# Optimization experiments

Hardware: AMD Instinct MI355X
Metric: run time of the kernel (lower is better)

Reference implementation:

```python
import jax, jax.numpy as jnp
import numpy as np

TEMP = 11.313708498984761  # sqrt(head_dim=128)

def setup_inputs() -> dict:
    key = jax.random.key(0)
    kq, kk, kv, km = jax.random.split(key, 4)
    B, H, S, D = 2, 16, 2048, 128
    q = jax.random.normal(kq, (B, H, S, D), dtype=jnp.float32)
    k = jax.random.normal(kk, (B, H, S, D), dtype=jnp.float32)
    v = jax.random.normal(kv, (B, H, S, D), dtype=jnp.float32)
    mask = jax.random.randint(km, (B, 1, S, S), 0, 2, dtype=jnp.int32)
    return {"q": q, "k": k, "v": v, "mask": mask}

def reference(q, k, v, mask):
    # atten = (q / temp) @ k^T  -> [B,H,S,S]
    atten = jnp.einsum("bhsd,bhtd->bhst", q / TEMP, k)
    maskf = mask.astype(atten.dtype)
    # torch masked_fill_(mask.bool(), 1e-9): positions where mask != 0 get 1e-9
    atten = jnp.where(mask.astype(bool), jnp.asarray(1e-9, atten.dtype), atten)
    atten = jax.nn.softmax(atten, axis=-1)
    # then multiply by mask (zeros out mask==0 positions)
    atten = atten * maskf
    # dropout: eval mode (identity) for a deterministic correctness baseline
    out = jnp.einsum("bhst,bhtd->bhsd", atten, v)
    return (out, atten)
```

## Files before the change

### kernel.cpp

```cpp
#include <hip/hip_runtime.h>
#include <stdint.h>

#define B_ 2
#define H_ 16
#define S_ 2048
#define D_ 128

typedef float f32x4 __attribute__((ext_vector_type(4)));
typedef float f32x16 __attribute__((ext_vector_type(16)));
typedef short bf16x8 __attribute__((ext_vector_type(8)));
typedef unsigned short u16x4 __attribute__((ext_vector_type(4)));
typedef int i32x4 __attribute__((ext_vector_type(4)));

__device__ __forceinline__ unsigned short f2bf(float x){
  union { float f; uint32_t u; } c; c.f = x;
  uint32_t u = c.u;
  uint32_t r = (u + 0x7FFFu + ((u >> 16) & 1u)) >> 16;
  return (unsigned short)r;
}

__device__ __forceinline__ void gload_lds16(const void* g, void* l){
  __builtin_amdgcn_global_load_lds(
      (const __attribute__((address_space(1))) unsigned int*)g,
      (__attribute__((address_space(3))) unsigned int*)l, 16, 0, 0);
}

__global__ void prep_kernel(const float* __restrict__ k, const float* __restrict__ v,
                            const int* __restrict__ mask,
                            unsigned short* __restrict__ KB, unsigned short* __restrict__ VT,
                            unsigned long long* __restrict__ bits){
  __shared__ float tile[64][73];
  const int blk = blockIdx.x;
  const int tid = threadIdx.x;
  if (blk < 8192){
    size_t i = (size_t)blk * 256 + tid;
    f32x4 val = __builtin_nontemporal_load(&((const f32x4*)k)[i]);
    u16x4 o; o[0]=f2bf(val.x); o[1]=f2bf(val.y); o[2]=f2bf(val.z); o[3]=f2bf(val.w);
    __builtin_nontemporal_store(o, &((u16x4*)KB)[i]);
  } else if (blk < 10240){
    int b2 = blk - 8192;
    int bh = b2 >> 6;
    int ts = (b2 >> 1) & 31;
    int dsec = b2 & 1;
    int t0 = ts*64, d0 = dsec*64;
    const float* vb = v + ((size_t)bh*S_ + t0)*D_ + d0;
    #pragma unroll
    for (int i=0;i<4;++i){
      int fi = i*256 + tid;
      int r = fi >> 4;
      int c4 = (fi & 15) * 4;
      f32x4 val = __builtin_nontemporal_load((const f32x4*)(vb + (size_t)r*D_ + c4));
      tile[r][c4+0]=val.x; tile[r][c4+1]=val.y; tile[r][c4+2]=val.z; tile[r][c4+3]=val.w;
    }
    __syncthreads();
    unsigned short* ob = VT + ((size_t)bh*D_ + d0)*S_ + t0;
    #pragma unroll
    for (int i=0;i<4;++i){
      int ui = i*256 + tid;
      int dr = ui >> 4;
      int tc = (ui & 15) * 4;
      u16x4 o;
      o[0] = f2bf(tile[tc+0][dr]);
      o[1] = f2bf(tile[tc+1][dr]);
      o[2] = f2bf(tile[tc+2][dr]);
      o[3] = f2bf(tile[tc+3][dr]);
      __builtin_nontemporal_store(o, (u16x4*)(ob + (size_t)dr*S_ + tc));
    }
  } else {
    int row = blk - 10240;
    const int* mrow = mask + (size_t)row*S_;
    int w = tid >> 6;
    int lane = tid & 63;
    #pragma unroll
    for (int i=0;i<8;++i){
      int t = i*256 + tid;
      unsigned long long bm = __ballot(__builtin_nontemporal_load(&mrow[t]) != 0);
      if (lane == 0) bits[(size_t)row*32 + i*4 + w] = bm;
    }
  }
}

__launch_bounds__(512, 4)
__global__ void fused_kernel(const float* __restrict__ q,
                             const unsigned long long* __restrict__ bits,
                             const unsigned short* __restrict__ KB,
                             const unsigned short* __restrict__ VT,
                             float* __restrict__ outp,
                             float* __restrict__ atten)
{
  __shared__ __align__(16) unsigned char Ksm[2][16384];
  __shared__ __align__(16) unsigned char Vsm[2][16384];
  __shared__ float lred[8][32];
  const int tid = threadIdx.x;
  const int lane = tid & 63;
  const int w = tid >> 6;
  const int l32 = lane & 31;
  const int lh = lane >> 5;

  const int orig = blockIdx.x;
  const int blk = (orig & 7) * 64 + (orig >> 3);
  const int bh = blk >> 4;
  const int qt = blk & 15;
  const int b = bh >> 4;
  const int s0 = qt * 128;
  const int r = w >> 1;
  const int cQ = w & 1;
  const int qrow = s0 + 32*r + l32;

  const float QS = 1.4426950408889634f / 11.313708498984761f;

  bf16x8 qf[8];
  {
    const float* qp = q + ((size_t)bh*S_ + qrow)*D_ + 8*lh;
    #pragma unroll
    for (int m=0; m<8; ++m){
      f32x4 a0 = __builtin_nontemporal_load((const f32x4*)(qp + 16*m));
      f32x4 a1 = __builtin_nontemporal_load((const f32x4*)(qp + 16*m + 4));
      bf16x8 f;
      f[0]=(short)f2bf(a0.x*QS); f[1]=(short)f2bf(a0.y*QS);
      f[2]=(short)f2bf(a0.z*QS); f[3]=(short)f2bf(a0.w*QS);
      f[4]=(short)f2bf(a1.x*QS); f[5]=(short)f2bf(a1.y*QS);
      f[6]=(short)f2bf(a1.z*QS); f[7]=(short)f2bf(a1.w*QS);
      qf[m] = f;
    }
  }

  f32x16 Wacc[2];
  #pragma unroll
  for (int n=0;n<2;++n)
    #pragma unroll
    for (int e=0;e<16;++e) Wacc[n][e] = 0.f;
  float lsum = 0.f;

  const unsigned char* Kgb = (const unsigned char*)(KB + (size_t)bh*S_*D_);
  const unsigned char* Vgb = (const unsigned char*)(VT + (size_t)bh*D_*S_);
  const unsigned long long* bitsb = bits + (size_t)b*S_*32 + (size_t)qrow*32;

  uint32_t koff[2], voff[2];
  int kbase[2];
  {
    int lq = lane >> 4, ls = lane & 15;
    #pragma unroll
    for (int i=0;i<2;++i){
      int c = 2*w + i;
      kbase[i] = c*1024;
      int rr = c*4 + lq;
      int ss = ls ^ (rr & 15);
      koff[i] = (uint32_t)(rr*256 + ss*16);
      int d  = rr*2 + (ss>>3);
      int ts = ss & 7;
      voff[i] = (uint32_t)(d*(S_*2) + ts*16);
    }
  }

  unsigned long long mbn = bitsb[0];
  #pragma unroll
  for (int i=0;i<2;++i){
    gload_lds16(Kgb + koff[i], &Ksm[0][kbase[i]]);
    gload_lds16(Vgb + voff[i], &Vsm[0][kbase[i]]);
  }

  int cur = 0;
  for (int it=0; it<32; ++it){
    asm volatile("s_waitcnt vmcnt(0)" ::: "memory");
    __builtin_amdgcn_sched_barrier(0);
    __builtin_amdgcn_s_barrier();
    __builtin_amdgcn_sched_barrier(0);

    unsigned long long mb = mbn;
    if (it+1 < 32){
      mbn = bitsb[it+1];
      const unsigned char* Kp = Kgb + (size_t)(it+1)*16384;
      const unsigned char* Vp = Vgb + (size_t)(it+1)*128;
      #pragma unroll
      for (int i=0;i<2;++i){
        gload_lds16(Kp + koff[i], &Ksm[cur^1][kbase[i]]);
        gload_lds16(Vp + voff[i], &Vsm[cur^1][kbase[i]]);
      }
      __builtin_amdgcn_sched_barrier(0);
    }

    f32x16 Sacc;
    #pragma unroll
    for (int e=0;e<16;++e) Sacc[e] = 0.f;
    const int trow = 32*cQ + l32;
    const unsigned char* kb = &Ksm[cur][trow*256];
    const int txr = trow & 15;
    __builtin_amdgcn_s_setprio(1);
    #pragma unroll
    for (int m=0; m<8; ++m){
      int slot = (2*m + lh) ^ txr;
      bf16x8 kf = *(const bf16x8*)(kb + (slot<<4));
      Sacc = __builtin_amdgcn_mfma_f32_32x32x16_bf16(kf, qf[m], Sacc, 0,0,0);
    }
    __builtin_amdgcn_s_setprio(0);

    uint32_t mw = (uint32_t)(mb >> (32*cQ + 4*lh));
    #pragma unroll
    for (int reg=0; reg<16; ++reg){
      const int tb = (reg&3) + 8*(reg>>2);
      float x = ((mw >> tb) & 1u) ? 0.f : Sacc[reg];
      lsum += __builtin_amdgcn_exp2f(x);
    }

    unsigned long long ms = mb >> (8*lh);
    uint32_t mlo = (uint32_t)ms, mhi = (uint32_t)(ms >> 32);
    #pragma unroll
    for (int m2=0; m2<4; ++m2){
      uint32_t bt = ((m2 < 2 ? mlo : mhi) >> (16*(m2&1))) & 0xFFu;
      union { bf16x8 v; uint32_t u[4]; } pk;
      #pragma unroll
      for (int j2=0; j2<4; ++j2){
        pk.u[j2] = (((bt>>(2*j2))&1u) ? 0x3F80u : 0u)
                 | (((bt>>(2*j2+1))&1u) ? 0x3F800000u : 0u);
      }
      __builtin_amdgcn_s_setprio(1);
      #pragma unroll
      for (int n=0; n<2; ++n){
        const int dd = 32*(2*cQ + n) + l32;
        int slot = ((((dd&1)<<3) | (2*m2 + lh)) ^ ((dd>>1)&15));
        bf16x8 vf = *(const bf16x8*)(&Vsm[cur][(dd>>1)*256 + (slot<<4)]);
        Wacc[n] = __builtin_amdgcn_mfma_f32_32x32x16_bf16(pk.v, vf, Wacc[n], 0,0,0);
      }
      __builtin_amdgcn_s_setprio(0);
    }
    cur ^= 1;
  }

  lsum += __shfl_xor(lsum, 32);
  if (lane < 32) lred[w][l32] = lsum;
  __syncthreads();

  unsigned long long* bitlds = (unsigned long long*)&Ksm[0][0];
  float* csm = (float*)&Vsm[0][0];
  {
    const i32x4* bsrc = (const i32x4*)(bits + ((size_t)b*S_ + s0)*32);
    i32x4* bdst = (i32x4*)bitlds;
    #pragma unroll
    for (int i=0;i<4;++i)
      bdst[i*512 + tid] = bsrc[i*512 + tid];
    if (tid < 128){
      int rr = tid >> 5;
      csm[tid] = 1.0f / (lred[2*rr][tid&31] + lred[2*rr+1][tid&31]);
    }
  }

  #pragma unroll
  for (int reg=0; reg<16; ++reg){
    int crow = (reg&3) + 8*(reg>>2) + 4*lh;
    float cv = 1.0f / (lred[2*r][crow] + lred[2*r+1][crow]);
    int row = s0 + 32*r + crow;
    #pragma unroll
    for (int n=0; n<2; ++n){
      const int dd = 32*(2*cQ + n) + l32;
      __builtin_nontemporal_store(cv*Wacc[n][reg],
                                  &outp[((size_t)bh*S_ + row)*D_ + dd]);
    }
  }

  __syncthreads();

  {
    f32x4* abase = (f32x4*)(atten + ((size_t)bh*S_ + s0)*S_);
    const int word = tid >> 4;
    const int sh = (tid & 15)*4;
    for (int j=0; j<128; ++j){
      float c = csm[j];
      unsigned long long wv = bitlds[j*32 + word];
      uint32_t nib = (uint32_t)(wv >> sh) & 0xFu;
      f32x4 o = { (nib&1u)?c:0.f, (nib&2u)?c:0.f, (nib&4u)?c:0.f, (nib&8u)?c:0.f };
      __builtin_nontemporal_store(o, &abase[j*512 + tid]);
    }
  }
}

extern "C" void kernel_launch(void* const* d_in, const int* in_sizes, int n_in,
                              void* d_out, int out_size, void* d_ws, size_t ws_size,
                              hipStream_t stream){
  const float* q = (const float*)d_in[0];
  const float* k = (const float*)d_in[1];
  const float* v = (const float*)d_in[2];
  const int* mask = (const int*)d_in[3];
  float* outp = (float*)d_out;
  float* atten = outp + (size_t)B_*H_*S_*D_;

  unsigned short* KB = (unsigned short*)d_ws;
  unsigned short* VT = KB + (size_t)B_*H_*S_*D_;
  unsigned long long* bits = (unsigned long long*)(VT + (size_t)B_*H_*S_*D_);

  hipLaunchKernelGGL(prep_kernel,  dim3(14336), dim3(256), 0, stream, k, v, mask, KB, VT, bits);
  hipLaunchKernelGGL(fused_kernel, dim3(512),   dim3(512), 0, stream, q, bits, KB, VT, outp, atten);
}
```

Measured before the change: 223.1 us.

## Split into row-sum pass and PV pass interleaved with attention-matrix stores

The single QK+PV loop becomes two passes. The first streams only K tiles and accumulates the masked exp2 row sums. The second streams only V tiles, runs the PV MFMAs and writes the corresponding four rows of the dense attention output each iteration, so the large store stream overlaps with compute instead of running as a serial tail. The row normalisers are computed once into shared memory before the second pass. A relaxed vmcnt wait lets the just-issued stores stay in flight across the barrier. The trade-offs are an extra pass over the mask bits and more barriers.

```diff
diff --git a/kernel.cpp b/kernel.cpp
--- a/kernel.cpp
+++ b/kernel.cpp
@@ -91,6 +91,7 @@
   __shared__ __align__(16) unsigned char Ksm[2][16384];
   __shared__ __align__(16) unsigned char Vsm[2][16384];
   __shared__ float lred[8][32];
+  __shared__ float csm[128];
   const int tid = threadIdx.x;
   const int lane = tid & 63;
   const int w = tid >> 6;
@@ -125,11 +126,6 @@
     }
   }
 
-  f32x16 Wacc[2];
-  #pragma unroll
-  for (int n=0;n<2;++n)
-    #pragma unroll
-    for (int e=0;e<16;++e) Wacc[n][e] = 0.f;
   float lsum = 0.f;
 
   const unsigned char* Kgb = (const unsigned char*)(KB + (size_t)bh*S_*D_);
@@ -155,10 +151,8 @@
 
   unsigned long long mbn = bitsb[0];
   #pragma unroll
-  for (int i=0;i<2;++i){
+  for (int i=0;i<2;++i)
     gload_lds16(Kgb + koff[i], &Ksm[0][kbase[i]]);
-    gload_lds16(Vgb + voff[i], &Vsm[0][kbase[i]]);
-  }
 
   int cur = 0;
   for (int it=0; it<32; ++it){
@@ -171,12 +165,9 @@
     if (it+1 < 32){
       mbn = bitsb[it+1];
       const unsigned char* Kp = Kgb + (size_t)(it+1)*16384;
-      const unsigned char* Vp = Vgb + (size_t)(it+1)*128;
       #pragma unroll
-      for (int i=0;i<2;++i){
+      for (int i=0;i<2;++i)
         gload_lds16(Kp + koff[i], &Ksm[cur^1][kbase[i]]);
-        gload_lds16(Vp + voff[i], &Vsm[cur^1][kbase[i]]);
-      }
       __builtin_amdgcn_sched_barrier(0);
     }
 
@@ -201,6 +192,52 @@
       const int tb = (reg&3) + 8*(reg>>2);
       float x = ((mw >> tb) & 1u) ? 0.f : Sacc[reg];
       lsum += __builtin_amdgcn_exp2f(x);
+    }
+    cur ^= 1;
+  }
+
+  lsum += __shfl_xor(lsum, 32);
+  if (lane < 32) lred[w][l32] = lsum;
+  __syncthreads();
+  if (tid < 128){
+    int rr = tid >> 5;
+    csm[tid] = 1.0f / (lred[2*rr][tid&31] + lred[2*rr+1][tid&31]);
+  }
+
+  unsigned long long* bitlds = (unsigned long long*)&Ksm[0][0];
+  {
+    const i32x4* bsrc = (const i32x4*)(bits + ((size_t)b*S_ + s0)*32);
+    i32x4* bdst = (i32x4*)bitlds;
+    #pragma unroll
+    for (int i=0;i<4;++i)
+      bdst[i*512 + tid] = bsrc[i*512 + tid];
+  }
+  unsigned long long mb2n = bitsb[0];
+  #pragma unroll
+  for (int i=0;i<2;++i)
+    gload_lds16(Vgb + voff[i], &Vsm[0][kbase[i]]);
+  __syncthreads();
+
+  f32x16 Wacc[2];
+  #pragma unroll
+  for (int n=0;n<2;++n)
+    #pragma unroll
+    for (int e=0;e<16;++e) Wacc[n][e] = 0.f;
+
+  f32x4* abase = (f32x4*)(atten + ((size_t)bh*S_ + s0)*S_);
+  const int aword = tid >> 4;
+  const int ash = (tid & 15)*4;
+
+  cur = 0;
+  for (int it=0; it<32; ++it){
+    unsigned long long mb = mb2n;
+    if (it+1 < 32){
+      mb2n = bitsb[it+1];
+      const unsigned char* Vp = Vgb + (size_t)(it+1)*128;
+      #pragma unroll
+      for (int i=0;i<2;++i)
+        gload_lds16(Vp + voff[i], &Vsm[cur^1][kbase[i]]);
+      __builtin_amdgcn_sched_barrier(0);
     }
 
     unsigned long long ms = mb >> (8*lh);
@@ -224,52 +261,37 @@
       }
       __builtin_amdgcn_s_setprio(0);
     }
+
+    #pragma unroll
+    for (int sub=0; sub<4; ++sub){
+      int j = 4*it + sub;
+      float c = csm[j];
+      unsigned long long wv = bitlds[j*32 + aword];
+      uint32_t nib = (uint32_t)(wv >> ash) & 0xFu;
+      f32x4 o = { (nib&1u)?c:0.f, (nib&2u)?c:0.f, (nib&4u)?c:0.f, (nib&8u)?c:0.f };
+      __builtin_nontemporal_store(o, &abase[j*512 + tid]);
+    }
+
+    if (it+1 < 32){
+      __builtin_amdgcn_sched_barrier(0);
+      asm volatile("s_waitcnt vmcnt(4)" ::: "memory");
+      __builtin_amdgcn_sched_barrier(0);
+      __builtin_amdgcn_s_barrier();
+      __builtin_amdgcn_sched_barrier(0);
+    }
     cur ^= 1;
-  }
-
-  lsum += __shfl_xor(lsum, 32);
-  if (lane < 32) lred[w][l32] = lsum;
-  __syncthreads();
-
-  unsigned long long* bitlds = (unsigned long long*)&Ksm[0][0];
-  float* csm = (float*)&Vsm[0][0];
-  {
-    const i32x4* bsrc = (const i32x4*)(bits + ((size_t)b*S_ + s0)*32);
-    i32x4* bdst = (i32x4*)bitlds;
-    #pragma unroll
-    for (int i=0;i<4;++i)
-      bdst[i*512 + tid] = bsrc[i*512 + tid];
-    if (tid < 128){
-      int rr = tid >> 5;
-      csm[tid] = 1.0f / (lred[2*rr][tid&31] + lred[2*rr+1][tid&31]);
-    }
   }
 
   #pragma unroll
   for (int reg=0; reg<16; ++reg){
     int crow = (reg&3) + 8*(reg>>2) + 4*lh;
-    float cv = 1.0f / (lred[2*r][crow] + lred[2*r+1][crow]);
+    float cv = csm[32*r + crow];
     int row = s0 + 32*r + crow;
     #pragma unroll
     for (int n=0; n<2; ++n){
       const int dd = 32*(2*cQ + n) + l32;
       __builtin_nontemporal_store(cv*Wacc[n][reg],
                                   &outp[((size_t)bh*S_ + row)*D_ + dd]);
-    }
-  }
-
-  __syncthreads();
-
-  {
-    f32x4* abase = (f32x4*)(atten + ((size_t)bh*S_ + s0)*S_);
-    const int word = tid >> 4;
-    const int sh = (tid & 15)*4;
-    for (int j=0; j<128; ++j){
-      float c = csm[j];
-      unsigned long long wv = bitlds[j*32 + word];
-      uint32_t nib = (uint32_t)(wv >> sh) & 0xFu;
-      f32x4 o = { (nib&1u)?c:0.f, (nib&2u)?c:0.f, (nib&4u)?c:0.f, (nib&8u)?c:0.f };
-      __builtin_nontemporal_store(o, &abase[j*512 + tid]);
     }
   }
 }
```

Measured after the change: 261.3 us. 1.17x slower.
